# Kernel tuning notes

Hardware: AMD Instinct MI355X
Metric: run time of the kernel (lower is better)

## Reference

```python
import jax, jax.numpy as jnp
import numpy as np

B, T, F, E = 256, 100, 34, 1024


def setup_inputs() -> dict:
    key = jax.random.key(0)
    ks = jax.random.split(key, 12)
    sc = 1.0 / np.sqrt(E)
    u = lambda k, shape: jax.random.uniform(k, shape, jnp.float32, -sc, sc)
    return {
        "x": jax.random.normal(ks[0], (B, T, F), jnp.float32),
        "W_lin": u(ks[1], (E, F)),
        "b_lin": u(ks[2], (E,)),
        "W_ih1": u(ks[3], (4 * E, E)),
        "W_hh1": u(ks[4], (4 * E, E)),
        "b_ih1": u(ks[5], (4 * E,)),
        "b_hh1": u(ks[6], (4 * E,)),
        "W_ih2": u(ks[7], (4 * E, E)),
        "W_hh2": u(ks[8], (4 * E, E)),
        "b_ih2": u(ks[9], (4 * E,)),
        "b_hh2": u(ks[10], (4 * E,)),
    }


def _gate_update(gates, c):
    # torch LSTMCell gate order: input, forget, cell(g), output
    i, f, g, o = jnp.split(gates, 4, axis=-1)
    c_new = jax.nn.sigmoid(f) * c + jax.nn.sigmoid(i) * jnp.tanh(g)
    h_new = jax.nn.sigmoid(o) * jnp.tanh(c_new)
    return h_new, c_new


def reference(x, W_lin, b_lin, W_ih1, W_hh1, b_ih1, b_hh1, W_ih2, W_hh2, b_ih2, b_hh2):
    hd = W_hh1.shape[1]
    bsz = x.shape[0]
    enc = x @ W_lin.T + b_lin                      # [B,T,E]
    # Precompute layer-1 input projections (incl. both biases) for all timesteps
    xg1 = jnp.einsum('bte,ge->btg', enc, W_ih1) + (b_ih1 + b_hh1)  # [B,T,4E]
    xs = jnp.swapaxes(xg1, 0, 1)                   # [T,B,4E] time-major for scan
    b2 = b_ih2 + b_hh2
    z = jnp.zeros((bsz, hd), jnp.float32)

    def step(carry, xg):
        h1, c1, h2, c2 = carry
        h1, c1 = _gate_update(xg + h1 @ W_hh1.T, c1)
        h2, c2 = _gate_update(h1 @ W_ih2.T + b2 + h2 @ W_hh2.T, c2)
        return (h1, c1, h2, c2), None

    (h1, c1, h2, c2), _ = jax.lax.scan(step, (z, z, z, z), xs)
    return (h2, c2)
```

## Files before the change

### kernel.cpp

```cpp
#include <hip/hip_runtime.h>

#define USH unsigned short
#define AGENT __HIP_MEMORY_SCOPE_AGENT
typedef __attribute__((ext_vector_type(8))) short short8;
typedef __attribute__((ext_vector_type(4))) float f32x4;

__device__ __forceinline__ USH rne_bf16(float f){
  unsigned int u = __float_as_uint(f);
  u = (u + 0x7fffu + ((u >> 16) & 1u)) >> 16;
  return (USH)u;
}
__device__ __forceinline__ float sigm(float x){ return 1.f / (1.f + __expf(-x)); }
__device__ __forceinline__ float tanh_(float x){ return 1.f - 2.f / (__expf(2.f * x) + 1.f); }
__device__ __forceinline__ void gload16(const void* g, void* l){
  __builtin_amdgcn_global_load_lds((const __attribute__((address_space(1))) unsigned int*)g,
                                   (__attribute__((address_space(3))) unsigned int*)l, 16, 0, 0);
}
__device__ __forceinline__ void st_bf16_sc1(USH* p, USH v){
  asm volatile("global_store_short %0, %1, off sc1" :: "v"(p), "v"((unsigned int)v) : "memory");
}
#define MFMA __builtin_amdgcn_mfma_f32_16x16x32_bf16

__device__ __forceinline__ void waitflags(const int* f, int tA, int tB, int l){
  const int* q = f + ((l < 32) ? (l * 4) : (128 + (l - 32) * 4));
  const int tgt = (l < 32) ? tA : tB;
  for (;;){
    int v0 = __hip_atomic_load(q + 0, __ATOMIC_RELAXED, AGENT);
    int v1 = __hip_atomic_load(q + 1, __ATOMIC_RELAXED, AGENT);
    int v2 = __hip_atomic_load(q + 2, __ATOMIC_RELAXED, AGENT);
    int v3 = __hip_atomic_load(q + 3, __ATOMIC_RELAXED, AGENT);
    int m = min(min(v0, v1), min(v2, v3));
    if (__all(m >= tgt)) return;
    __builtin_amdgcn_s_sleep(1);
  }
}

__global__ void k_fold(const float* __restrict__ Wih1, const float* __restrict__ Wlin,
                       const float* __restrict__ blin, const float* __restrict__ bih1,
                       const float* __restrict__ bhh1, USH* __restrict__ Wcpk, float* __restrict__ bc){
  const int n = blockIdx.x;
  const int t = threadIdx.x;
  float a[34];
#pragma unroll
  for (int f = 0; f < 34; ++f) a[f] = 0.f;
  float ab = 0.f;
  for (int e = t; e < 1024; e += 64){
    const float wv = Wih1[n * 1024 + e];
    ab += wv * blin[e];
    const float* wl = Wlin + e * 34;
#pragma unroll
    for (int f = 0; f < 34; ++f) a[f] += wv * wl[f];
  }
#pragma unroll
  for (int off = 32; off > 0; off >>= 1){
    ab += __shfl_down(ab, off);
#pragma unroll
    for (int f = 0; f < 34; ++f) a[f] += __shfl_down(a[f], off);
  }
  if (t == 0){
    const int nc = n & 1023, gq = n >> 10, cgi = nc >> 4, lp = nc & 15;
    for (int f = 0; f < 64; ++f){
      const float v = (f < 34) ? a[f] : 0.f;
      const int lane = lp + (((f >> 3) & 3) << 4);
      const int idx = (((cgi * 2 + (f >> 5)) * 4 + gq) * 64 + lane) * 8 + (f & 7);
      Wcpk[idx] = rne_bf16(v);
    }
    bc[n] = ab + bih1[n] + bhh1[n];
  }
}

__global__ void k_pack(const float* __restrict__ Whh1, const float* __restrict__ Wih2,
                       const float* __restrict__ Whh2, const float* __restrict__ bih2,
                       const float* __restrict__ bhh2,
                       USH* __restrict__ P1, USH* __restrict__ P2a, USH* __restrict__ P2b,
                       float* __restrict__ ob2){
  const int N = 4096 * 1024;
  for (int i = blockIdx.x * blockDim.x + threadIdx.x; i < N; i += gridDim.x * blockDim.x){
    const int j = i & 7, li = (i >> 3) & 63, gq = (i >> 9) & 3, ks = (i >> 11) & 31, cgi = i >> 16;
    const int n = gq * 1024 + cgi * 16 + (li & 15);
    const int k = ks * 32 + ((li >> 4) << 3) + j;
    const int src = n * 1024 + k;
    P1[i]  = rne_bf16(Whh1[src]);
    P2a[i] = rne_bf16(Wih2[src]);
    P2b[i] = rne_bf16(Whh2[src]);
    if (i < 4096) ob2[i] = bih2[i] + bhh2[i];
  }
}

__global__ void k_xpk(const float* __restrict__ x, USH* __restrict__ xp){
  const int N = 100 * 16384;
  for (int i = blockIdx.x * blockDim.x + threadIdx.x; i < N; i += gridDim.x * blockDim.x){
    const int j = i & 7, li = (i >> 3) & 63, ks = (i >> 9) & 1, g = (i >> 10) & 15, t = i >> 14;
    const int row = g * 16 + (li & 15);
    const int f = ks * 32 + ((li >> 4) << 3) + j;
    xp[i] = (f < 34) ? rne_bf16(x[(row * 100 + t) * 34 + f]) : (USH)0;
  }
}

__global__ __launch_bounds__(256) void k_persist(
    USH* __restrict__ hA1, USH* __restrict__ hA2, int* __restrict__ flags,
    const USH* __restrict__ Wpk1, const USH* __restrict__ Wpk2a, const USH* __restrict__ Wpk2b,
    const USH* __restrict__ Wcpk, const USH* __restrict__ xpk,
    const float* __restrict__ bc, const float* __restrict__ b2, float* __restrict__ out,
    int d1, int d2, int useFence)
{
  __shared__ __attribute__((aligned(16))) char lds[131072];
  const int tid = threadIdx.x, w = tid >> 6, l = tid & 63;
  const int wg = blockIdx.x;
  const int isL2 = wg >> 7;
  const int cg = (wg & 127) >> 1;
  const int mh = wg & 1;
  const int gb = mh * 8 + w * 2;
  const int col = cg * 16 + (l & 15);
  const int lofs16 = l * 16;
  const int lofs8 = l * 8;

  const int ks2 = cg >> 1;
  const int l16 = (cg * 2 + ((l & 15) >> 3)) & 3;
  const int j2 = l & 7;

  float creg[2][4];
#pragma unroll
  for (int mf = 0; mf < 2; ++mf)
#pragma unroll
    for (int r = 0; r < 4; ++r) creg[mf][r] = 0.f;

  if (!isL2){
    const USH* s = Wpk1 + (size_t)cg * 65536;
#pragma unroll
    for (int r = 0; r < 32; ++r)
      gload16(s + (r * 4 + w) * 512 + lofs8, &lds[(r * 4 + w) * 1024]);
    short8 wc[2][4];
#pragma unroll
    for (int ks = 0; ks < 2; ++ks)
#pragma unroll
      for (int gq = 0; gq < 4; ++gq)
        wc[ks][gq] = *(const short8*)(Wcpk + (size_t)cg * 4096 + (ks * 4 + gq) * 512 + lofs8);
    __syncthreads();
    const float bi0 = bc[col], bi1 = bc[1024 + col], bi2 = bc[2048 + col], bi3 = bc[3072 + col];

    for (int p = 0; p < 100; ++p){
      if (p >= 1){
        if (tid < 64){
          waitflags(flags, p, useFence ? (p - 2) : -1, tid);
          if (useFence && tid == 0) __builtin_amdgcn_fence(__ATOMIC_ACQUIRE, "agent");
        }
        __syncthreads();
      }
      f32x4 acc[2][4];
#pragma unroll
      for (int mf = 0; mf < 2; ++mf)
#pragma unroll
        for (int gq = 0; gq < 4; ++gq) acc[mf][gq] = (f32x4){0.f, 0.f, 0.f, 0.f};

      if (p > 0){
        const USH* Ap = hA1 + (size_t)((p - 1) % d1) * 262144 + gb * 16384 + lofs8;
#pragma unroll
        for (int ks = 0; ks < 32; ++ks){
          short8 a0 = *(const short8*)(Ap + ks * 512);
          short8 a1 = *(const short8*)(Ap + 16384 + ks * 512);
          const char* bb = &lds[ks * 4096 + lofs16];
#pragma unroll
          for (int gq = 0; gq < 4; ++gq){
            short8 bf = *(const short8*)(bb + gq * 1024);
            acc[0][gq] = MFMA(a0, bf, acc[0][gq], 0, 0, 0);
            acc[1][gq] = MFMA(a1, bf, acc[1][gq], 0, 0, 0);
          }
        }
      }
      const USH* Xp = xpk + (size_t)p * 16384 + gb * 1024 + lofs8;
#pragma unroll
      for (int ks = 0; ks < 2; ++ks){
        short8 a0 = *(const short8*)(Xp + ks * 512);
        short8 a1 = *(const short8*)(Xp + 1024 + ks * 512);
#pragma unroll
        for (int gq = 0; gq < 4; ++gq){
          acc[0][gq] = MFMA(a0, wc[ks][gq], acc[0][gq], 0, 0, 0);
          acc[1][gq] = MFMA(a1, wc[ks][gq], acc[1][gq], 0, 0, 0);
        }
      }
      USH* hn = hA1 + (size_t)(p % d1) * 262144;
#pragma unroll
      for (int mf = 0; mf < 2; ++mf){
        const int g2 = gb + mf;
#pragma unroll
        for (int r = 0; r < 4; ++r){
          const float gi = acc[mf][0][r] + bi0;
          const float gf = acc[mf][1][r] + bi1;
          const float gg = acc[mf][2][r] + bi2;
          const float go = acc[mf][3][r] + bi3;
          const float cn = sigm(gf) * creg[mf][r] + sigm(gi) * tanh_(gg);
          creg[mf][r] = cn;
          const int lane2 = ((l >> 4) << 2) + r + (l16 << 4);
          st_bf16_sc1(&hn[(g2 * 32 + ks2) * 512 + lane2 * 8 + j2], rne_bf16(sigm(go) * tanh_(cn)));
        }
      }
      asm volatile("s_waitcnt vmcnt(0)" ::: "memory");
      __syncthreads();
      if (tid == 0){
        if (useFence) __builtin_amdgcn_fence(__ATOMIC_RELEASE, "agent");
        __hip_atomic_store(&flags[wg], p + 1, __ATOMIC_RELAXED, AGENT);
      }
    }
  } else {
    const USH* s = Wpk2b + (size_t)cg * 65536;
#pragma unroll
    for (int r = 0; r < 24; ++r)
      gload16(s + (r * 4 + w) * 512 + lofs8, &lds[(r * 4 + w) * 1024]);
    __syncthreads();
    const float bi0 = b2[col], bi1 = b2[1024 + col], bi2 = b2[2048 + col], bi3 = b2[3072 + col];
    const USH* Wsa = Wpk2a + (size_t)cg * 65536;
    const USH* Wsb = Wpk2b + (size_t)cg * 65536;

    for (int p = 1; p <= 100; ++p){
#pragma unroll
      for (int r = 0; r < 4; ++r)
        gload16(Wsa + (r * 4 + w) * 512 + lofs8, &lds[98304 + (r * 4 + w) * 1024]);
      if (tid < 64){
        waitflags(flags, p, p - 1, tid);
        if (useFence && tid == 0) __builtin_amdgcn_fence(__ATOMIC_ACQUIRE, "agent");
      }
      __syncthreads();

      const USH* A1p = hA1 + (size_t)((p - 1) % d1) * 262144 + gb * 16384 + lofs8;
      const USH* A2p = hA2 + (size_t)((p - 1) % d2) * 262144 + gb * 16384 + lofs8;

      f32x4 acc[2][4];
#pragma unroll
      for (int mf = 0; mf < 2; ++mf)
#pragma unroll
        for (int gq = 0; gq < 4; ++gq) acc[mf][gq] = (f32x4){0.f, 0.f, 0.f, 0.f};

      short8 ar[2][8];
#pragma unroll
      for (int kk = 0; kk < 4; ++kk){
        ar[0][kk * 2]     = *(const short8*)(A1p + kk * 512);
        ar[0][kk * 2 + 1] = *(const short8*)(A1p + 16384 + kk * 512);
      }
#pragma unroll
      for (int c = 0; c < 10; ++c){
        if (c) __syncthreads();
        if (c < 9){
          const int t = c + 1;
          const USH* src = (t < 8) ? (Wsa + t * 8192) : (Wsb + (t - 2) * 8192);
          char* dst = &lds[98304 + (t & 1) * 16384];
#pragma unroll
          for (int r = 0; r < 4; ++r)
            gload16(src + (r * 4 + w) * 512 + lofs8, dst + (r * 4 + w) * 1024);
          const USH* Ab = (t < 8) ? A1p : A2p;
          const int ksb = (t < 8) ? t * 4 : (t - 2) * 4;
#pragma unroll
          for (int kk = 0; kk < 4; ++kk){
            ar[t & 1][kk * 2]     = *(const short8*)(Ab + (ksb + kk) * 512);
            ar[t & 1][kk * 2 + 1] = *(const short8*)(Ab + 16384 + (ksb + kk) * 512);
          }
        }
        const int rb = (c < 8) ? 2 * c : 16 + 4 * (c - 8);
        const int rn = (c < 8) ? 2 : 4;
        short8 ra[4][2];
#pragma unroll
        for (int q = 0; q < 4; ++q){
          if (q < rn){
            ra[q][0] = *(const short8*)(A2p + (rb + q) * 512);
            ra[q][1] = *(const short8*)(A2p + 16384 + (rb + q) * 512);
          }
        }
        const char* cb = &lds[98304 + (c & 1) * 16384 + lofs16];
#pragma unroll
        for (int kk = 0; kk < 4; ++kk){
#pragma unroll
          for (int gq = 0; gq < 4; ++gq){
            short8 bf = *(const short8*)(cb + kk * 4096 + gq * 1024);
            acc[0][gq] = MFMA(ar[c & 1][kk * 2],     bf, acc[0][gq], 0, 0, 0);
            acc[1][gq] = MFMA(ar[c & 1][kk * 2 + 1], bf, acc[1][gq], 0, 0, 0);
          }
        }
#pragma unroll
        for (int q = 0; q < 4; ++q){
          if (q < rn){
            const char* bb = &lds[(rb + q) * 4096 + lofs16];
#pragma unroll
            for (int gq = 0; gq < 4; ++gq){
              short8 bf = *(const short8*)(bb + gq * 1024);
              acc[0][gq] = MFMA(ra[q][0], bf, acc[0][gq], 0, 0, 0);
              acc[1][gq] = MFMA(ra[q][1], bf, acc[1][gq], 0, 0, 0);
            }
          }
        }
      }

      if (p < 100){
        USH* hn = hA2 + (size_t)(p % d2) * 262144;
#pragma unroll
        for (int mf = 0; mf < 2; ++mf){
          const int g2 = gb + mf;
#pragma unroll
          for (int r = 0; r < 4; ++r){
            const float gi = acc[mf][0][r] + bi0;
            const float gf = acc[mf][1][r] + bi1;
            const float gg = acc[mf][2][r] + bi2;
            const float go = acc[mf][3][r] + bi3;
            const float cn = sigm(gf) * creg[mf][r] + sigm(gi) * tanh_(gg);
            creg[mf][r] = cn;
            const int lane2 = ((l >> 4) << 2) + r + (l16 << 4);
            st_bf16_sc1(&hn[(g2 * 32 + ks2) * 512 + lane2 * 8 + j2], rne_bf16(sigm(go) * tanh_(cn)));
          }
        }
      } else {
#pragma unroll
        for (int mf = 0; mf < 2; ++mf){
#pragma unroll
          for (int r = 0; r < 4; ++r){
            const int row = (gb + mf) * 16 + ((l >> 4) << 2) + r;
            const float gi = acc[mf][0][r] + bi0;
            const float gf = acc[mf][1][r] + bi1;
            const float gg = acc[mf][2][r] + bi2;
            const float go = acc[mf][3][r] + bi3;
            const float cn = sigm(gf) * creg[mf][r] + sigm(gi) * tanh_(gg);
            out[row * 1024 + col] = sigm(go) * tanh_(cn);
            out[262144 + row * 1024 + col] = cn;
          }
        }
      }
      asm volatile("s_waitcnt vmcnt(0)" ::: "memory");
      __syncthreads();
      if (tid == 0){
        if (useFence) __builtin_amdgcn_fence(__ATOMIC_RELEASE, "agent");
        __hip_atomic_store(&flags[wg], p, __ATOMIC_RELAXED, AGENT);
      }
    }
  }
}

extern "C" void kernel_launch(void* const* d_in, const int* in_sizes, int n_in,
                              void* d_out, int out_size, void* d_ws, size_t ws_size,
                              hipStream_t stream){
  const float* x    = (const float*)d_in[0];
  const float* Wlin = (const float*)d_in[1];
  const float* blin = (const float*)d_in[2];
  const float* Wih1 = (const float*)d_in[3];
  const float* Whh1 = (const float*)d_in[4];
  const float* bih1 = (const float*)d_in[5];
  const float* bhh1 = (const float*)d_in[6];
  const float* Wih2 = (const float*)d_in[7];
  const float* Whh2 = (const float*)d_in[8];
  const float* bih2 = (const float*)d_in[9];
  const float* bhh2 = (const float*)d_in[10];
  char* ws = (char*)d_ws;

  const size_t SLOT = 524288;
  int d1 = 100, d2 = 100, useFence = 0;
  const size_t need = 1024 + 200 * SLOT + 3 * 8388608ull + 524288 + 3276800 + 32768;
  if (ws_size < need){ d1 = 3; d2 = 2; useFence = 1; }

  size_t off = 0;
  int*   flags = (int*)(ws + off);  off = 1024;
  USH*   hA2   = (USH*)(ws + off);  off += (size_t)d2 * SLOT;
  USH*   hA1   = (USH*)(ws + off);  off += (size_t)d1 * SLOT;
  USH*   Wpk1  = (USH*)(ws + off);  off += 8388608;
  USH*   Wpk2a = (USH*)(ws + off);  off += 8388608;
  USH*   Wpk2b = (USH*)(ws + off);  off += 8388608;
  USH*   Wcpk  = (USH*)(ws + off);  off += 524288;
  USH*   xpk   = (USH*)(ws + off);  off += 3276800;
  float* bc    = (float*)(ws + off); off += 16384;
  float* b2    = (float*)(ws + off);

  hipMemsetAsync(ws, 0, 1024 + SLOT, stream);
  k_fold<<<4096, 64, 0, stream>>>(Wih1, Wlin, blin, bih1, bhh1, Wcpk, bc);
  k_pack<<<2048, 256, 0, stream>>>(Whh1, Wih2, Whh2, bih2, bhh2, Wpk1, Wpk2a, Wpk2b, b2);
  k_xpk<<<1024, 256, 0, stream>>>(x, xpk);

  float* outp = (float*)d_out;
  void* args[] = {&hA1, &hA2, &flags, &Wpk1, &Wpk2a, &Wpk2b, &Wcpk, &xpk, &bc, &b2, &outp,
                  &d1, &d2, &useFence};
  hipError_t e = hipLaunchCooperativeKernel((void*)k_persist, dim3(256), dim3(256), args, 0, stream);
  if (e != hipSuccess){
    k_persist<<<dim3(256), dim3(256), 0, stream>>>(hA1, hA2, flags, Wpk1, Wpk2a, Wpk2b,
                                                   Wcpk, xpk, bc, b2, outp, d1, d2, useFence);
  }
}
```

Before: 1.980 ms.

## Precompute layer-2 input projection one step ahead, keep full W_hh2 in LDS

Layer-2 workgroups now compute the h1·W_ih2 contribution for the next timestep right after publishing their own h2. This takes it off the critical path that waits on h2 from the previous step. The full W_hh2 slice (32 rows) is now held resident in LDS. W_ih2 is read straight from global memory instead of being double-buffered through LDS, which removes the per-chunk syncthreads. The cost is more global reads of W_ih2 each step and an extra flag wait and sync per step. The flag semantics also shift, since h2 is published before the next h1 projection is computed.

```diff
diff --git a/kernel.cpp b/kernel.cpp
--- a/kernel.cpp
+++ b/kernel.cpp
@@ -141,10 +141,8 @@
 
     for (int p = 0; p < 100; ++p){
       if (p >= 1){
-        if (tid < 64){
-          waitflags(flags, p, useFence ? (p - 2) : -1, tid);
-          if (useFence && tid == 0) __builtin_amdgcn_fence(__ATOMIC_ACQUIRE, "agent");
-        }
+        if (tid < 64) waitflags(flags, p, useFence ? (p - 2) : -1, tid);
+        if (useFence && tid == 0) __builtin_amdgcn_fence(__ATOMIC_ACQUIRE, "agent");
         __syncthreads();
       }
       f32x4 acc[2][4];
@@ -205,87 +203,52 @@
   } else {
     const USH* s = Wpk2b + (size_t)cg * 65536;
 #pragma unroll
-    for (int r = 0; r < 24; ++r)
+    for (int r = 0; r < 32; ++r)
       gload16(s + (r * 4 + w) * 512 + lofs8, &lds[(r * 4 + w) * 1024]);
     __syncthreads();
     const float bi0 = b2[col], bi1 = b2[1024 + col], bi2 = b2[2048 + col], bi3 = b2[3072 + col];
-    const USH* Wsa = Wpk2a + (size_t)cg * 65536;
-    const USH* Wsb = Wpk2b + (size_t)cg * 65536;
+    const USH* Bw = Wpk2a + (size_t)cg * 65536;
+
+    f32x4 accP[2][4];
+#pragma unroll
+    for (int mf = 0; mf < 2; ++mf)
+#pragma unroll
+      for (int gq = 0; gq < 4; ++gq) accP[mf][gq] = (f32x4){0.f, 0.f, 0.f, 0.f};
+
+    if (tid < 64) waitflags(flags, 1, -1, tid);
+    if (useFence && tid == 0) __builtin_amdgcn_fence(__ATOMIC_ACQUIRE, "agent");
+    __syncthreads();
+    {
+      const USH* A1p = hA1 + gb * 16384 + lofs8;
+#pragma unroll
+      for (int ks = 0; ks < 32; ++ks){
+        short8 a0 = *(const short8*)(A1p + ks * 512);
+        short8 a1 = *(const short8*)(A1p + 16384 + ks * 512);
+#pragma unroll
+        for (int gq = 0; gq < 4; ++gq){
+          short8 bf = *(const short8*)(Bw + ks * 2048 + gq * 512 + lofs8);
+          accP[0][gq] = MFMA(a0, bf, accP[0][gq], 0, 0, 0);
+          accP[1][gq] = MFMA(a1, bf, accP[1][gq], 0, 0, 0);
+        }
+      }
+    }
 
     for (int p = 1; p <= 100; ++p){
-#pragma unroll
-      for (int r = 0; r < 4; ++r)
-        gload16(Wsa + (r * 4 + w) * 512 + lofs8, &lds[98304 + (r * 4 + w) * 1024]);
-      if (tid < 64){
-        waitflags(flags, p, p - 1, tid);
-        if (useFence && tid == 0) __builtin_amdgcn_fence(__ATOMIC_ACQUIRE, "agent");
-      }
+      if (tid < 64) waitflags(flags, -1, p - 1, tid);
+      if (useFence && tid == 0) __builtin_amdgcn_fence(__ATOMIC_ACQUIRE, "agent");
       __syncthreads();
 
-      const USH* A1p = hA1 + (size_t)((p - 1) % d1) * 262144 + gb * 16384 + lofs8;
       const USH* A2p = hA2 + (size_t)((p - 1) % d2) * 262144 + gb * 16384 + lofs8;
-
-      f32x4 acc[2][4];
-#pragma unroll
-      for (int mf = 0; mf < 2; ++mf)
-#pragma unroll
-        for (int gq = 0; gq < 4; ++gq) acc[mf][gq] = (f32x4){0.f, 0.f, 0.f, 0.f};
-
-      short8 ar[2][8];
-#pragma unroll
-      for (int kk = 0; kk < 4; ++kk){
-        ar[0][kk * 2]     = *(const short8*)(A1p + kk * 512);
-        ar[0][kk * 2 + 1] = *(const short8*)(A1p + 16384 + kk * 512);
-      }
-#pragma unroll
-      for (int c = 0; c < 10; ++c){
-        if (c) __syncthreads();
-        if (c < 9){
-          const int t = c + 1;
-          const USH* src = (t < 8) ? (Wsa + t * 8192) : (Wsb + (t - 2) * 8192);
-          char* dst = &lds[98304 + (t & 1) * 16384];
-#pragma unroll
-          for (int r = 0; r < 4; ++r)
-            gload16(src + (r * 4 + w) * 512 + lofs8, dst + (r * 4 + w) * 1024);
-          const USH* Ab = (t < 8) ? A1p : A2p;
-          const int ksb = (t < 8) ? t * 4 : (t - 2) * 4;
-#pragma unroll
-          for (int kk = 0; kk < 4; ++kk){
-            ar[t & 1][kk * 2]     = *(const short8*)(Ab + (ksb + kk) * 512);
-            ar[t & 1][kk * 2 + 1] = *(const short8*)(Ab + 16384 + (ksb + kk) * 512);
-          }
-        }
-        const int rb = (c < 8) ? 2 * c : 16 + 4 * (c - 8);
-        const int rn = (c < 8) ? 2 : 4;
-        short8 ra[4][2];
-#pragma unroll
-        for (int q = 0; q < 4; ++q){
-          if (q < rn){
-            ra[q][0] = *(const short8*)(A2p + (rb + q) * 512);
-            ra[q][1] = *(const short8*)(A2p + 16384 + (rb + q) * 512);
-          }
-        }
-        const char* cb = &lds[98304 + (c & 1) * 16384 + lofs16];
-#pragma unroll
-        for (int kk = 0; kk < 4; ++kk){
-#pragma unroll
-          for (int gq = 0; gq < 4; ++gq){
-            short8 bf = *(const short8*)(cb + kk * 4096 + gq * 1024);
-            acc[0][gq] = MFMA(ar[c & 1][kk * 2],     bf, acc[0][gq], 0, 0, 0);
-            acc[1][gq] = MFMA(ar[c & 1][kk * 2 + 1], bf, acc[1][gq], 0, 0, 0);
-          }
-        }
-#pragma unroll
-        for (int q = 0; q < 4; ++q){
-          if (q < rn){
-            const char* bb = &lds[(rb + q) * 4096 + lofs16];
-#pragma unroll
-            for (int gq = 0; gq < 4; ++gq){
-              short8 bf = *(const short8*)(bb + gq * 1024);
-              acc[0][gq] = MFMA(ra[q][0], bf, acc[0][gq], 0, 0, 0);
-              acc[1][gq] = MFMA(ra[q][1], bf, acc[1][gq], 0, 0, 0);
-            }
-          }
+#pragma unroll
+      for (int ks = 0; ks < 32; ++ks){
+        short8 a0 = *(const short8*)(A2p + ks * 512);
+        short8 a1 = *(const short8*)(A2p + 16384 + ks * 512);
+        const char* bb = &lds[ks * 4096 + lofs16];
+#pragma unroll
+        for (int gq = 0; gq < 4; ++gq){
+          short8 bf = *(const short8*)(bb + gq * 1024);
+          accP[0][gq] = MFMA(a0, bf, accP[0][gq], 0, 0, 0);
+          accP[1][gq] = MFMA(a1, bf, accP[1][gq], 0, 0, 0);
         }
       }
 
@@ -296,37 +259,62 @@
           const int g2 = gb + mf;
 #pragma unroll
           for (int r = 0; r < 4; ++r){
-            const float gi = acc[mf][0][r] + bi0;
-            const float gf = acc[mf][1][r] + bi1;
-            const float gg = acc[mf][2][r] + bi2;
-            const float go = acc[mf][3][r] + bi3;
+            const float gi = accP[mf][0][r] + bi0;
+            const float gf = accP[mf][1][r] + bi1;
+            const float gg = accP[mf][2][r] + bi2;
+            const float go = accP[mf][3][r] + bi3;
             const float cn = sigm(gf) * creg[mf][r] + sigm(gi) * tanh_(gg);
             creg[mf][r] = cn;
             const int lane2 = ((l >> 4) << 2) + r + (l16 << 4);
             st_bf16_sc1(&hn[(g2 * 32 + ks2) * 512 + lane2 * 8 + j2], rne_bf16(sigm(go) * tanh_(cn)));
           }
         }
+        asm volatile("s_waitcnt vmcnt(0)" ::: "memory");
+        __syncthreads();
+        if (tid == 0){
+          if (useFence) __builtin_amdgcn_fence(__ATOMIC_RELEASE, "agent");
+          __hip_atomic_store(&flags[wg], p, __ATOMIC_RELAXED, AGENT);
+        }
+
+        if (tid < 64) waitflags(flags, p + 1, -1, tid);
+        if (useFence && tid == 0) __builtin_amdgcn_fence(__ATOMIC_ACQUIRE, "agent");
+        __syncthreads();
+        f32x4 accQ[2][4];
+#pragma unroll
+        for (int mf = 0; mf < 2; ++mf)
+#pragma unroll
+          for (int gq = 0; gq < 4; ++gq) accQ[mf][gq] = (f32x4){0.f, 0.f, 0.f, 0.f};
+        const USH* A1p = hA1 + (size_t)(p % d1) * 262144 + gb * 16384 + lofs8;
+#pragma unroll
+        for (int ks = 0; ks < 32; ++ks){
+          short8 a0 = *(const short8*)(A1p + ks * 512);
+          short8 a1 = *(const short8*)(A1p + 16384 + ks * 512);
+#pragma unroll
+          for (int gq = 0; gq < 4; ++gq){
+            short8 bf = *(const short8*)(Bw + ks * 2048 + gq * 512 + lofs8);
+            accQ[0][gq] = MFMA(a0, bf, accQ[0][gq], 0, 0, 0);
+            accQ[1][gq] = MFMA(a1, bf, accQ[1][gq], 0, 0, 0);
+          }
+        }
+#pragma unroll
+        for (int mf = 0; mf < 2; ++mf)
+#pragma unroll
+          for (int gq = 0; gq < 4; ++gq) accP[mf][gq] = accQ[mf][gq];
       } else {
 #pragma unroll
         for (int mf = 0; mf < 2; ++mf){
 #pragma unroll
           for (int r = 0; r < 4; ++r){
             const int row = (gb + mf) * 16 + ((l >> 4) << 2) + r;
-            const float gi = acc[mf][0][r] + bi0;
-            const float gf = acc[mf][1][r] + bi1;
-            const float gg = acc[mf][2][r] + bi2;
-            const float go = acc[mf][3][r] + bi3;
+            const float gi = accP[mf][0][r] + bi0;
+            const float gf = accP[mf][1][r] + bi1;
+            const float gg = accP[mf][2][r] + bi2;
+            const float go = accP[mf][3][r] + bi3;
             const float cn = sigm(gf) * creg[mf][r] + sigm(gi) * tanh_(gg);
             out[row * 1024 + col] = sigm(go) * tanh_(cn);
             out[262144 + row * 1024 + col] = cn;
           }
         }
-      }
-      asm volatile("s_waitcnt vmcnt(0)" ::: "memory");
-      __syncthreads();
-      if (tid == 0){
-        if (useFence) __builtin_amdgcn_fence(__ATOMIC_RELEASE, "agent");
-        __hip_atomic_store(&flags[wg], p, __ATOMIC_RELAXED, AGENT);
       }
     }
   }
```

After: 3.397 ms. 1.72x slower.

## Split layer-2 wait into per-half dependency phases with padded flags

Applied to the files above, without the earlier changes.

Each workgroup's flag is padded to its own 16-byte slot, and waiters now poll only the 64 producers of their batch half instead of all 128 groups. Layer 2 first computes the W_ih2·h1 part as soon as layer-1 flags are ready, then waits for layer-2 flags before the W_hh2·h2 part, so the recurrent-state dependency is waited on later. The final step no longer publishes a flag, and the A-operand prefetch and register double-buffering are simplified into direct loads, which may expose more load latency.

```diff
diff --git a/kernel.cpp b/kernel.cpp
--- a/kernel.cpp
+++ b/kernel.cpp
@@ -21,16 +21,11 @@
 }
 #define MFMA __builtin_amdgcn_mfma_f32_16x16x32_bf16
 
-__device__ __forceinline__ void waitflags(const int* f, int tA, int tB, int l){
-  const int* q = f + ((l < 32) ? (l * 4) : (128 + (l - 32) * 4));
-  const int tgt = (l < 32) ? tA : tB;
+__device__ __forceinline__ void waitgrp(const int* f, int grpbase, int mh, int tgt, int l){
+  const int* q = f + (grpbase + l * 2 + mh) * 4;
   for (;;){
-    int v0 = __hip_atomic_load(q + 0, __ATOMIC_RELAXED, AGENT);
-    int v1 = __hip_atomic_load(q + 1, __ATOMIC_RELAXED, AGENT);
-    int v2 = __hip_atomic_load(q + 2, __ATOMIC_RELAXED, AGENT);
-    int v3 = __hip_atomic_load(q + 3, __ATOMIC_RELAXED, AGENT);
-    int m = min(min(v0, v1), min(v2, v3));
-    if (__all(m >= tgt)) return;
+    int v = __hip_atomic_load(q, __ATOMIC_RELAXED, AGENT);
+    if (__all(v >= tgt)) return;
     __builtin_amdgcn_s_sleep(1);
   }
 }
@@ -114,7 +109,6 @@
   const int col = cg * 16 + (l & 15);
   const int lofs16 = l * 16;
   const int lofs8 = l * 8;
-
   const int ks2 = cg >> 1;
   const int l16 = (cg * 2 + ((l & 15) >> 3)) & 3;
   const int j2 = l & 7;
@@ -142,9 +136,10 @@
     for (int p = 0; p < 100; ++p){
       if (p >= 1){
         if (tid < 64){
-          waitflags(flags, p, useFence ? (p - 2) : -1, tid);
-          if (useFence && tid == 0) __builtin_amdgcn_fence(__ATOMIC_ACQUIRE, "agent");
-        }
+          waitgrp(flags, 0, mh, p, l);
+          if (useFence) waitgrp(flags, 128, mh, p - 2, l);
+        }
+        if (useFence && tid == 0) __builtin_amdgcn_fence(__ATOMIC_ACQUIRE, "agent");
         __syncthreads();
       }
       f32x4 acc[2][4];
@@ -152,7 +147,6 @@
       for (int mf = 0; mf < 2; ++mf)
 #pragma unroll
         for (int gq = 0; gq < 4; ++gq) acc[mf][gq] = (f32x4){0.f, 0.f, 0.f, 0.f};
-
       if (p > 0){
         const USH* Ap = hA1 + (size_t)((p - 1) % d1) * 262144 + gb * 16384 + lofs8;
 #pragma unroll
@@ -199,27 +193,24 @@
       __syncthreads();
       if (tid == 0){
         if (useFence) __builtin_amdgcn_fence(__ATOMIC_RELEASE, "agent");
-        __hip_atomic_store(&flags[wg], p + 1, __ATOMIC_RELAXED, AGENT);
+        __hip_atomic_store(&flags[wg * 4], p + 1, __ATOMIC_RELAXED, AGENT);
       }
     }
   } else {
-    const USH* s = Wpk2b + (size_t)cg * 65536;
+    const USH* Wsa = Wpk2a + (size_t)cg * 65536;
+    const USH* Wsb = Wpk2b + (size_t)cg * 65536;
 #pragma unroll
     for (int r = 0; r < 24; ++r)
-      gload16(s + (r * 4 + w) * 512 + lofs8, &lds[(r * 4 + w) * 1024]);
+      gload16(Wsb + (r * 4 + w) * 512 + lofs8, &lds[(r * 4 + w) * 1024]);
     __syncthreads();
     const float bi0 = b2[col], bi1 = b2[1024 + col], bi2 = b2[2048 + col], bi3 = b2[3072 + col];
-    const USH* Wsa = Wpk2a + (size_t)cg * 65536;
-    const USH* Wsb = Wpk2b + (size_t)cg * 65536;
 
     for (int p = 1; p <= 100; ++p){
 #pragma unroll
       for (int r = 0; r < 4; ++r)
         gload16(Wsa + (r * 4 + w) * 512 + lofs8, &lds[98304 + (r * 4 + w) * 1024]);
-      if (tid < 64){
-        waitflags(flags, p, p - 1, tid);
-        if (useFence && tid == 0) __builtin_amdgcn_fence(__ATOMIC_ACQUIRE, "agent");
-      }
+      if (tid < 64) waitgrp(flags, 0, mh, p, l);
+      if (useFence && tid == 0) __builtin_amdgcn_fence(__ATOMIC_ACQUIRE, "agent");
       __syncthreads();
 
       const USH* A1p = hA1 + (size_t)((p - 1) % d1) * 262144 + gb * 16384 + lofs8;
@@ -231,61 +222,62 @@
 #pragma unroll
         for (int gq = 0; gq < 4; ++gq) acc[mf][gq] = (f32x4){0.f, 0.f, 0.f, 0.f};
 
-      short8 ar[2][8];
-#pragma unroll
-      for (int kk = 0; kk < 4; ++kk){
-        ar[0][kk * 2]     = *(const short8*)(A1p + kk * 512);
-        ar[0][kk * 2 + 1] = *(const short8*)(A1p + 16384 + kk * 512);
-      }
-#pragma unroll
-      for (int c = 0; c < 10; ++c){
-        if (c) __syncthreads();
-        if (c < 9){
-          const int t = c + 1;
-          const USH* src = (t < 8) ? (Wsa + t * 8192) : (Wsb + (t - 2) * 8192);
-          char* dst = &lds[98304 + (t & 1) * 16384];
+#pragma unroll
+      for (int c = 0; c < 8; ++c){
+        if (c < 7){
+          const USH* src = Wsa + (c + 1) * 8192;
+          char* dst = &lds[98304 + ((c + 1) & 1) * 16384];
 #pragma unroll
           for (int r = 0; r < 4; ++r)
             gload16(src + (r * 4 + w) * 512 + lofs8, dst + (r * 4 + w) * 1024);
-          const USH* Ab = (t < 8) ? A1p : A2p;
-          const int ksb = (t < 8) ? t * 4 : (t - 2) * 4;
-#pragma unroll
-          for (int kk = 0; kk < 4; ++kk){
-            ar[t & 1][kk * 2]     = *(const short8*)(Ab + (ksb + kk) * 512);
-            ar[t & 1][kk * 2 + 1] = *(const short8*)(Ab + 16384 + (ksb + kk) * 512);
-          }
-        }
-        const int rb = (c < 8) ? 2 * c : 16 + 4 * (c - 8);
-        const int rn = (c < 8) ? 2 : 4;
-        short8 ra[4][2];
-#pragma unroll
-        for (int q = 0; q < 4; ++q){
-          if (q < rn){
-            ra[q][0] = *(const short8*)(A2p + (rb + q) * 512);
-            ra[q][1] = *(const short8*)(A2p + 16384 + (rb + q) * 512);
-          }
         }
         const char* cb = &lds[98304 + (c & 1) * 16384 + lofs16];
 #pragma unroll
         for (int kk = 0; kk < 4; ++kk){
+          short8 a0 = *(const short8*)(A1p + (c * 4 + kk) * 512);
+          short8 a1 = *(const short8*)(A1p + 16384 + (c * 4 + kk) * 512);
 #pragma unroll
           for (int gq = 0; gq < 4; ++gq){
             short8 bf = *(const short8*)(cb + kk * 4096 + gq * 1024);
-            acc[0][gq] = MFMA(ar[c & 1][kk * 2],     bf, acc[0][gq], 0, 0, 0);
-            acc[1][gq] = MFMA(ar[c & 1][kk * 2 + 1], bf, acc[1][gq], 0, 0, 0);
+            acc[0][gq] = MFMA(a0, bf, acc[0][gq], 0, 0, 0);
+            acc[1][gq] = MFMA(a1, bf, acc[1][gq], 0, 0, 0);
           }
         }
-#pragma unroll
-        for (int q = 0; q < 4; ++q){
-          if (q < rn){
-            const char* bb = &lds[(rb + q) * 4096 + lofs16];
-#pragma unroll
-            for (int gq = 0; gq < 4; ++gq){
-              short8 bf = *(const short8*)(bb + gq * 1024);
-              acc[0][gq] = MFMA(ra[q][0], bf, acc[0][gq], 0, 0, 0);
-              acc[1][gq] = MFMA(ra[q][1], bf, acc[1][gq], 0, 0, 0);
-            }
-          }
+        __syncthreads();
+      }
+
+#pragma unroll
+      for (int r = 0; r < 4; ++r){
+        gload16(Wsb + 49152 + (r * 4 + w) * 512 + lofs8, &lds[98304  + (r * 4 + w) * 1024]);
+        gload16(Wsb + 57344 + (r * 4 + w) * 512 + lofs8, &lds[114688 + (r * 4 + w) * 1024]);
+      }
+
+      if (tid < 64) waitgrp(flags, 128, mh, p - 1, l);
+      if (useFence && tid == 0) __builtin_amdgcn_fence(__ATOMIC_ACQUIRE, "agent");
+      __syncthreads();
+
+#pragma unroll
+      for (int ks = 0; ks < 24; ++ks){
+        short8 a0 = *(const short8*)(A2p + ks * 512);
+        short8 a1 = *(const short8*)(A2p + 16384 + ks * 512);
+        const char* bb = &lds[ks * 4096 + lofs16];
+#pragma unroll
+        for (int gq = 0; gq < 4; ++gq){
+          short8 bf = *(const short8*)(bb + gq * 1024);
+          acc[0][gq] = MFMA(a0, bf, acc[0][gq], 0, 0, 0);
+          acc[1][gq] = MFMA(a1, bf, acc[1][gq], 0, 0, 0);
+        }
+      }
+#pragma unroll
+      for (int kk = 0; kk < 8; ++kk){
+        short8 a0 = *(const short8*)(A2p + (24 + kk) * 512);
+        short8 a1 = *(const short8*)(A2p + 16384 + (24 + kk) * 512);
+        const char* bb = &lds[98304 + kk * 4096 + lofs16];
+#pragma unroll
+        for (int gq = 0; gq < 4; ++gq){
+          short8 bf = *(const short8*)(bb + gq * 1024);
+          acc[0][gq] = MFMA(a0, bf, acc[0][gq], 0, 0, 0);
+          acc[1][gq] = MFMA(a1, bf, acc[1][gq], 0, 0, 0);
         }
       }
 
@@ -306,6 +298,12 @@
             st_bf16_sc1(&hn[(g2 * 32 + ks2) * 512 + lane2 * 8 + j2], rne_bf16(sigm(go) * tanh_(cn)));
           }
         }
+        asm volatile("s_waitcnt vmcnt(0)" ::: "memory");
+        __syncthreads();
+        if (tid == 0){
+          if (useFence) __builtin_amdgcn_fence(__ATOMIC_RELEASE, "agent");
+          __hip_atomic_store(&flags[wg * 4], p, __ATOMIC_RELAXED, AGENT);
+        }
       } else {
 #pragma unroll
         for (int mf = 0; mf < 2; ++mf){
@@ -321,12 +319,6 @@
             out[262144 + row * 1024 + col] = cn;
           }
         }
-      }
-      asm volatile("s_waitcnt vmcnt(0)" ::: "memory");
-      __syncthreads();
-      if (tid == 0){
-        if (useFence) __builtin_amdgcn_fence(__ATOMIC_RELEASE, "agent");
-        __hip_atomic_store(&flags[wg], p, __ATOMIC_RELAXED, AGENT);
       }
     }
   }
@@ -350,11 +342,11 @@
 
   const size_t SLOT = 524288;
   int d1 = 100, d2 = 100, useFence = 0;
-  const size_t need = 1024 + 200 * SLOT + 3 * 8388608ull + 524288 + 3276800 + 32768;
+  const size_t need = 4096 + 200 * SLOT + 3 * 8388608ull + 524288 + 3276800 + 32768;
   if (ws_size < need){ d1 = 3; d2 = 2; useFence = 1; }
 
   size_t off = 0;
-  int*   flags = (int*)(ws + off);  off = 1024;
+  int*   flags = (int*)(ws + off);  off = 4096;
   USH*   hA2   = (USH*)(ws + off);  off += (size_t)d2 * SLOT;
   USH*   hA1   = (USH*)(ws + off);  off += (size_t)d1 * SLOT;
   USH*   Wpk1  = (USH*)(ws + off);  off += 8388608;
@@ -365,7 +357,7 @@
   float* bc    = (float*)(ws + off); off += 16384;
   float* b2    = (float*)(ws + off);
 
-  hipMemsetAsync(ws, 0, 1024 + SLOT, stream);
+  hipMemsetAsync(ws, 0, 4096 + SLOT, stream);
   k_fold<<<4096, 64, 0, stream>>>(Wih1, Wlin, blin, bih1, bhh1, Wcpk, bc);
   k_pack<<<2048, 256, 0, stream>>>(Whh1, Wih2, Whh2, bih2, bhh2, Wpk1, Wpk2a, Wpk2b, b2);
   k_xpk<<<1024, 256, 0, stream>>>(x, xpk);
```

Result: slower. 2.660 ms (+34.4%).
